# Kernel optimization log

Measured on AMD Instinct MI355X. Metric: run time of the kernel, lower is better.

## Reference

```python
import jax, jax.numpy as jnp
import numpy as np

N_NODES = 50000
N_EDGES = 800000
IN_C = 256
HID_C = 256
OUT_C = 128
N_GRAPHS = 256


def setup_inputs() -> dict:
    key = jax.random.key(0)
    ks = jax.random.split(key, 12)
    x = jax.random.normal(ks[0], (N_NODES, IN_C), dtype=jnp.float32)
    src = jax.random.randint(ks[1], (N_EDGES,), 0, N_NODES, dtype=jnp.int32)
    dst = jnp.sort(jax.random.randint(ks[2], (N_EDGES,), 0, N_NODES, dtype=jnp.int32))
    p = jax.random.uniform(ks[3], (N_NODES,), dtype=jnp.float32)
    batch = jnp.sort(jax.random.randint(ks[4], (N_NODES,), 0, N_GRAPHS, dtype=jnp.int32))
    root_ptr = jax.random.randint(ks[5], (N_GRAPHS,), 0, N_NODES, dtype=jnp.int32)
    s1 = 1.0 / np.sqrt(IN_C)
    s2 = 1.0 / np.sqrt(HID_C)
    s3 = 1.0 / np.sqrt(2 * HID_C)
    Wl1 = jax.random.uniform(ks[6], (IN_C, HID_C), jnp.float32, -s1, s1)
    Wr1 = jax.random.uniform(ks[7], (IN_C, HID_C), jnp.float32, -s1, s1)
    b1 = jnp.zeros((HID_C,), jnp.float32)
    Wl2 = jax.random.uniform(ks[8], (HID_C, HID_C), jnp.float32, -s2, s2)
    Wr2 = jax.random.uniform(ks[9], (HID_C, HID_C), jnp.float32, -s2, s2)
    b2 = jnp.zeros((HID_C,), jnp.float32)
    Wlin = jax.random.uniform(ks[10], (2 * HID_C, OUT_C), jnp.float32, -s3, s3)
    blin = jax.random.uniform(ks[11], (OUT_C,), jnp.float32, -s3, s3)
    return {"x": x, "src": src, "dst": dst, "p": p, "batch": batch,
            "root_ptr": root_ptr, "num_graphs": N_GRAPHS,
            "Wl1": Wl1, "Wr1": Wr1, "b1": b1,
            "Wl2": Wl2, "Wr2": Wr2, "b2": b2,
            "Wlin": Wlin, "blin": blin}


def _sage_conv(x, src, dst, inv_deg, Wl, Wr, b):
    # mean aggregation of neighbor features: scatter-add then divide by degree
    agg = jax.ops.segment_sum(x[src], dst, num_segments=N_NODES)  # [N, d]
    agg = agg * inv_deg[:, None]
    return agg @ Wl + x @ Wr + b


def reference(x, src, dst, p, batch, root_ptr, num_graphs,
              Wl1, Wr1, b1, Wl2, Wr2, b2, Wlin, blin):
    # in-degree for mean aggregation (shared by both convs)
    deg = jax.ops.segment_sum(jnp.ones_like(dst, dtype=x.dtype), dst,
                              num_segments=N_NODES)
    inv_deg = jnp.where(deg > 0, 1.0 / jnp.maximum(deg, 1.0), 0.0)

    h = _sage_conv(x, src, dst, inv_deg, Wl1, Wr1, b1)
    h = jax.nn.relu(h)  # dropout is identity in eval mode
    h = _sage_conv(h, src, dst, inv_deg, Wl2, Wr2, b2)

    # masked mean pool of p-weighted features per graph
    pw = h * p[:, None]
    gsum = jax.ops.segment_sum(pw, batch, num_segments=num_graphs)
    gcnt = jax.ops.segment_sum(jnp.ones_like(p), batch, num_segments=num_graphs)
    gmean = gsum / jnp.maximum(gcnt, 1.0)[:, None]

    feat = jnp.concatenate([h[root_ptr], gmean], axis=-1)  # [G, 2*hid]
    return feat @ Wlin + blin
```

## Files before the change

kernel.cpp:

```cpp
#include <hip/hip_runtime.h>
#include <hip/hip_bf16.h>

#define N_NODES 50000
#define N_EDGES 800000
#define C_DIM   256
#define OUT_C   128
#define N_GRAPHS 256

typedef unsigned short ushort8 __attribute__((ext_vector_type(8)));
typedef __bf16         bf16x8  __attribute__((ext_vector_type(8)));
typedef float          f32x4   __attribute__((ext_vector_type(4)));

typedef __attribute__((address_space(1))) const unsigned int gu32;
typedef __attribute__((address_space(3))) unsigned int lu32;

#if __has_builtin(__builtin_amdgcn_sched_barrier)
#define SCHED_FENCE() __builtin_amdgcn_sched_barrier(0)
#else
#define SCHED_FENCE() ((void)0)
#endif

__device__ __forceinline__ float us2f(unsigned short u) {
    unsigned int x = ((unsigned int)u) << 16;
    return __builtin_bit_cast(float, x);
}
__device__ __forceinline__ unsigned short f2bf(float f) {
    unsigned int u = __builtin_bit_cast(unsigned int, f);
    u += 0x7fffu + ((u >> 16) & 1u);
    return (unsigned short)(u >> 16);
}

__device__ __forceinline__ int lower_bound_i(const int* __restrict__ a, int n, int v) {
    int lo = 0, hi = n;
    while (lo < hi) {
        int mid = (lo + hi) >> 1;
        if (a[mid] < v) lo = mid + 1; else hi = mid;
    }
    return lo;
}

__global__ void preprocess(const float* __restrict__ x, unsigned short* __restrict__ xb,
                           const float* __restrict__ W0, const float* __restrict__ W1,
                           const float* __restrict__ W2, const float* __restrict__ W3,
                           unsigned short* __restrict__ D0, unsigned short* __restrict__ D1,
                           unsigned short* __restrict__ D2, unsigned short* __restrict__ D3,
                           const int* __restrict__ dst, const int* __restrict__ batch,
                           int* __restrict__ row_ptr, int* __restrict__ graph_ptr,
                           float* __restrict__ inv_deg) {
    __shared__ float tile[64][65];
    int b = blockIdx.x;
    int t = threadIdx.x;
    if (b < 12500) {
        int i = b * 256 + t;
        float4 v = *(const float4*)(x + ((size_t)i << 2));
        ushort4 o;
        o.x = f2bf(v.x); o.y = f2bf(v.y); o.z = f2bf(v.z); o.w = f2bf(v.w);
        *(ushort4*)(xb + ((size_t)i << 2)) = o;
    } else if (b < 12564) {
        int b2 = b - 12500;
        const float* S; unsigned short* D;
        switch (b2 >> 4) {
            case 0: S = W0; D = D0; break;
            case 1: S = W1; D = D1; break;
            case 2: S = W2; D = D2; break;
            default: S = W3; D = D3; break;
        }
        int tl = b2 & 15;
        int kt = (tl >> 2) * 64, nt = (tl & 3) * 64;
#pragma unroll
        for (int j = 0; j < 16; ++j) {
            int idx = t + j * 256;
            int r = idx >> 6, c = idx & 63;
            tile[r][c] = S[(size_t)(kt + r) * 256 + nt + c];
        }
        __syncthreads();
#pragma unroll
        for (int j = 0; j < 16; ++j) {
            int idx = t + j * 256;
            int r = idx >> 6, c = idx & 63;
            D[(size_t)(nt + r) * 256 + kt + c] = f2bf(tile[c][r]);
        }
    } else {
        int i = (b - 12564) * 256 + t;
        if (i <= N_NODES) {
            int lb = lower_bound_i(dst, N_EDGES, i);
            row_ptr[i] = lb;
            if (i < N_NODES) {
                int ub = lower_bound_i(dst, N_EDGES, i + 1);
                int cnt = ub - lb;
                inv_deg[i] = (cnt > 0) ? (1.0f / (float)cnt) : 0.0f;
            }
        }
        if (i <= N_GRAPHS) graph_ptr[i] = lower_bound_i(batch, N_NODES, i);
    }
}

__global__ void aggregate(const unsigned short* __restrict__ X,
                          const int* __restrict__ src,
                          const int* __restrict__ row_ptr,
                          const float* __restrict__ inv_deg,
                          unsigned short* __restrict__ out) {
    int gw   = (blockIdx.x * blockDim.x + threadIdx.x) >> 6;
    int lane = threadIdx.x & 63;
    if (gw >= N_NODES) return;
    int e0 = row_ptr[gw], e1 = row_ptr[gw + 1];
    const int lo = lane << 2;
    float a0 = 0.f, a1 = 0.f, a2 = 0.f, a3 = 0.f;
    int e = e0;

    for (; e + 16 <= e1; e += 16) {
        ushort4 v[16];
#pragma unroll
        for (int j = 0; j < 16; ++j) {
            int s = __builtin_amdgcn_readfirstlane(src[e + j]);
            v[j] = *(const ushort4*)(X + ((size_t)s << 8) + lo);
        }
        SCHED_FENCE();
#pragma unroll
        for (int j = 0; j < 16; ++j) {
            a0 += us2f(v[j].x); a1 += us2f(v[j].y);
            a2 += us2f(v[j].z); a3 += us2f(v[j].w);
        }
    }
    int rem = e1 - e;
    if (rem > 0) {
        int cl = e1 - 1;
        ushort4 v[16]; float w[16];
#pragma unroll
        for (int j = 0; j < 16; ++j) {
            int ej = e + j;
            int ec = ej < cl ? ej : cl;
            w[j] = (ej < e1) ? 1.0f : 0.0f;
            int s = __builtin_amdgcn_readfirstlane(src[ec]);
            v[j] = *(const ushort4*)(X + ((size_t)s << 8) + lo);
        }
        SCHED_FENCE();
#pragma unroll
        for (int j = 0; j < 16; ++j) {
            a0 = fmaf(us2f(v[j].x), w[j], a0);
            a1 = fmaf(us2f(v[j].y), w[j], a1);
            a2 = fmaf(us2f(v[j].z), w[j], a2);
            a3 = fmaf(us2f(v[j].w), w[j], a3);
        }
    }

    float sc = inv_deg[gw];
    ushort4 o;
    o.x = f2bf(a0 * sc); o.y = f2bf(a1 * sc); o.z = f2bf(a2 * sc); o.w = f2bf(a3 * sc);
    *(ushort4*)(out + ((size_t)gw << 8) + lo) = o;
}

__global__ __launch_bounds__(512, 2)
void gemm_fused(const unsigned short* __restrict__ A1,
                const unsigned short* __restrict__ A2,
                const unsigned short* __restrict__ B1t,
                const unsigned short* __restrict__ B2t,
                const float* __restrict__ bias,
                unsigned short* __restrict__ C,
                int M, int do_relu) {
    __shared__ __align__(16) unsigned short As[8192];
    __shared__ __align__(16) unsigned short Bs[16384];

    const int t    = threadIdx.x;
    const int m0   = blockIdx.x * 128;
    const int lane = t & 63, wid = t >> 6;
    const int wm   = (wid >> 2) * 64;
    const int wn   = (wid & 3) * 64;
    const int lrow = lane & 15;
    const int kq   = lane >> 4;

    const f32x4 zero4 = {0.f, 0.f, 0.f, 0.f};
    f32x4 acc[4][4];
#pragma unroll
    for (int i = 0; i < 4; ++i)
#pragma unroll
        for (int j = 0; j < 4; ++j) acc[i][j] = zero4;

    for (int it = 0; it < 8; ++it) {
        const unsigned short* __restrict__ Ab = (it < 4) ? A1 : A2;
        const unsigned short* __restrict__ Bb = (it < 4) ? B1t : B2t;
        int ko = (it * 64) & 255;

#pragma unroll
        for (int i = 0; i < 2; ++i) {
            int q   = t + i * 512;
            int row = q >> 3;
            int kb  = (q & 7) ^ (row & 7);
            const unsigned short* ga = Ab + (size_t)(m0 + row) * 256 + ko + kb * 8;
            __builtin_amdgcn_global_load_lds((gu32*)ga, (lu32*)(As + q * 8), 16, 0, 0);
        }
#pragma unroll
        for (int i = 0; i < 4; ++i) {
            int q   = t + i * 512;
            int row = q >> 3;
            int kb  = (q & 7) ^ (row & 7);
            const unsigned short* gb = Bb + (size_t)row * 256 + ko + kb * 8;
            __builtin_amdgcn_global_load_lds((gu32*)gb, (lu32*)(Bs + q * 8), 16, 0, 0);
        }
        __syncthreads();

#pragma unroll
        for (int s = 0; s < 2; ++s) {
            int kqp = s * 4 + kq;
            bf16x8 af[4], bfr[4];
#pragma unroll
            for (int mi = 0; mi < 4; ++mi) {
                int r = wm + mi * 16 + lrow;
                int slot = r * 8 + (kqp ^ (lrow & 7));
                uint4 u = *(const uint4*)(As + slot * 8);
                af[mi] = __builtin_bit_cast(bf16x8, u);
            }
#pragma unroll
            for (int ni = 0; ni < 4; ++ni) {
                int r = wn + ni * 16 + lrow;
                int slot = r * 8 + (kqp ^ (lrow & 7));
                uint4 u = *(const uint4*)(Bs + slot * 8);
                bfr[ni] = __builtin_bit_cast(bf16x8, u);
            }
#pragma unroll
            for (int mi = 0; mi < 4; ++mi)
#pragma unroll
                for (int ni = 0; ni < 4; ++ni)
                    acc[mi][ni] = __builtin_amdgcn_mfma_f32_16x16x32_bf16(
                        af[mi], bfr[ni], acc[mi][ni], 0, 0, 0);
        }
        __syncthreads();
    }

    const int rbase = (lane >> 4) * 4;
#pragma unroll
    for (int ni = 0; ni < 4; ++ni) {
        int n  = wn + ni * 16 + lrow;
        float bv = bias[n];
#pragma unroll
        for (int mi = 0; mi < 4; ++mi) {
            int mb = m0 + wm + mi * 16 + rbase;
#pragma unroll
            for (int r = 0; r < 4; ++r) {
                int m = mb + r;
                if (m < M) {
                    float v = acc[mi][ni][r] + bv;
                    if (do_relu) v = fmaxf(v, 0.f);
                    C[(size_t)m * 256 + n] = f2bf(v);
                }
            }
        }
    }
}

__global__ void pool_final(const unsigned short* __restrict__ h2,
                           const float* __restrict__ p,
                           const int* __restrict__ graph_ptr,
                           const int* __restrict__ root_ptr,
                           const float* __restrict__ Wlin,
                           const float* __restrict__ blin,
                           float* __restrict__ out) {
    __shared__ float part[2][256];
    __shared__ float fl[512];
    int g = blockIdx.x;
    int t = threadIdx.x;
    int c = t & 255;
    int half = t >> 8;
    int s = graph_ptr[g], e = graph_ptr[g + 1];
    int mid = s + ((e - s) >> 1);
    int lo0 = half ? mid : s;
    int hi0 = half ? e : mid;

    float acc = 0.f;
    for (int n = lo0; n < hi0; n += 8) {
        int cl = hi0 - 1;
        float w[8]; unsigned short v[8];
#pragma unroll
        for (int j = 0; j < 8; ++j) {
            int nj = n + j;
            int ncj = nj < cl ? nj : cl;
            int nu = __builtin_amdgcn_readfirstlane(ncj);
            w[j] = (nj < hi0) ? p[nu] : 0.0f;
            v[j] = h2[(size_t)nu * 256 + c];
        }
        SCHED_FENCE();
#pragma unroll
        for (int j = 0; j < 8; ++j)
            acc = fmaf(us2f(v[j]), w[j], acc);
    }
    part[half][c] = acc;
    __syncthreads();

    if (half == 0) {
        float cnt = (float)(e - s);
        int root = root_ptr[g];
        fl[c]       = us2f(h2[(size_t)root * 256 + c]);
        fl[256 + c] = (part[0][c] + part[1][c]) / fmaxf(cnt, 1.0f);
    }
    __syncthreads();

    if (t < 128) {
        int o = t;
        float s0 = 0.f, s1 = 0.f, s2 = 0.f, s3 = 0.f;
        for (int k = 0; k < 512; k += 4) {
            s0 = fmaf(fl[k + 0], Wlin[(k + 0) * 128 + o], s0);
            s1 = fmaf(fl[k + 1], Wlin[(k + 1) * 128 + o], s1);
            s2 = fmaf(fl[k + 2], Wlin[(k + 2) * 128 + o], s2);
            s3 = fmaf(fl[k + 3], Wlin[(k + 3) * 128 + o], s3);
        }
        out[(size_t)g * 128 + o] = blin[o] + ((s0 + s1) + (s2 + s3));
    }
}

extern "C" void kernel_launch(void* const* d_in, const int* in_sizes, int n_in,
                              void* d_out, int out_size, void* d_ws, size_t ws_size,
                              hipStream_t stream) {
    const float* x        = (const float*)d_in[0];
    const int*   src      = (const int*)d_in[1];
    const int*   dst      = (const int*)d_in[2];
    const float* p        = (const float*)d_in[3];
    const int*   batch    = (const int*)d_in[4];
    const int*   root_ptr = (const int*)d_in[5];
    const float* Wl1  = (const float*)d_in[7];
    const float* Wr1  = (const float*)d_in[8];
    const float* b1   = (const float*)d_in[9];
    const float* Wl2  = (const float*)d_in[10];
    const float* Wr2  = (const float*)d_in[11];
    const float* b2   = (const float*)d_in[12];
    const float* Wlin = (const float*)d_in[13];
    const float* blin = (const float*)d_in[14];
    float* out = (float*)d_out;

    size_t off = 0;
    char* base = (char*)d_ws;
    auto alloc = [&](size_t bytes) -> void* {
        void* q = base + off;
        off += (bytes + 255) & ~(size_t)255;
        return q;
    };
    int*            row_ptr   = (int*)  alloc((N_NODES + 1) * sizeof(int));
    int*            graph_ptr = (int*)  alloc((N_GRAPHS + 1) * sizeof(int));
    float*          inv_deg   = (float*)alloc(N_NODES * sizeof(float));
    unsigned short* Wl1t = (unsigned short*)alloc(256 * 256 * 2);
    unsigned short* Wr1t = (unsigned short*)alloc(256 * 256 * 2);
    unsigned short* Wl2t = (unsigned short*)alloc(256 * 256 * 2);
    unsigned short* Wr2t = (unsigned short*)alloc(256 * 256 * 2);
    unsigned short* xb   = (unsigned short*)alloc((size_t)N_NODES * 256 * 2);
    unsigned short* aggb = (unsigned short*)alloc((size_t)N_NODES * 256 * 2);
    unsigned short* h1   = (unsigned short*)alloc((size_t)N_NODES * 256 * 2);
    unsigned short* h2   = (unsigned short*)alloc((size_t)N_NODES * 256 * 2);
    (void)ws_size; (void)n_in; (void)in_sizes; (void)out_size;

    preprocess<<<12760, 256, 0, stream>>>(x, xb, Wl1, Wr1, Wl2, Wr2,
                                          Wl1t, Wr1t, Wl2t, Wr2t,
                                          dst, batch, row_ptr, graph_ptr, inv_deg);

    dim3 ggrid((N_NODES + 127) / 128);

    aggregate<<<N_NODES / 4, 256, 0, stream>>>(xb, src, row_ptr, inv_deg, aggb);
    gemm_fused<<<ggrid, 512, 0, stream>>>(aggb, xb, Wl1t, Wr1t, b1, h1, N_NODES, 1);

    aggregate<<<N_NODES / 4, 256, 0, stream>>>(h1, src, row_ptr, inv_deg, aggb);
    gemm_fused<<<ggrid, 512, 0, stream>>>(aggb, h1, Wl2t, Wr2t, b2, h2, N_NODES, 0);

    pool_final<<<N_GRAPHS, 512, 0, stream>>>(h2, p, graph_ptr, root_ptr,
                                             Wlin, blin, out);
}
```

Baseline: 314.4 us.

## Fuse graph mean-pool into second GEMM epilogue via LDS and global atomics

The second SAGE GEMM epilogue now accumulates p-weighted outputs per graph into a small LDS buffer, then flushes them with global atomics into a zeroed gsum buffer. This removes the separate pass in pool_final that re-read all of h2. The x-conversion branch of preprocess now handles four vectors per thread, and extra blocks zero gsum. The fusion relies on each 128-row tile spanning at most 8 graphs, and it adds LDS atomic traffic and extra LDS usage to the GEMM epilogue.

```diff
diff --git a/kernel.cpp b/kernel.cpp
--- a/kernel.cpp
+++ b/kernel.cpp
@@ -7,7 +7,6 @@
 #define OUT_C   128
 #define N_GRAPHS 256
 
-typedef unsigned short ushort8 __attribute__((ext_vector_type(8)));
 typedef __bf16         bf16x8  __attribute__((ext_vector_type(8)));
 typedef float          f32x4   __attribute__((ext_vector_type(4)));
 
@@ -46,18 +45,22 @@
                            unsigned short* __restrict__ D2, unsigned short* __restrict__ D3,
                            const int* __restrict__ dst, const int* __restrict__ batch,
                            int* __restrict__ row_ptr, int* __restrict__ graph_ptr,
-                           float* __restrict__ inv_deg) {
+                           float* __restrict__ inv_deg, float* __restrict__ gsum) {
     __shared__ float tile[64][65];
     int b = blockIdx.x;
     int t = threadIdx.x;
-    if (b < 12500) {
-        int i = b * 256 + t;
-        float4 v = *(const float4*)(x + ((size_t)i << 2));
-        ushort4 o;
-        o.x = f2bf(v.x); o.y = f2bf(v.y); o.z = f2bf(v.z); o.w = f2bf(v.w);
-        *(ushort4*)(xb + ((size_t)i << 2)) = o;
-    } else if (b < 12564) {
-        int b2 = b - 12500;
+    if (b < 3125) {
+        int base = b * 1024 + t;
+#pragma unroll
+        for (int j = 0; j < 4; ++j) {
+            int i = base + j * 256;
+            float4 v = *(const float4*)(x + ((size_t)i << 2));
+            ushort4 o;
+            o.x = f2bf(v.x); o.y = f2bf(v.y); o.z = f2bf(v.z); o.w = f2bf(v.w);
+            *(ushort4*)(xb + ((size_t)i << 2)) = o;
+        }
+    } else if (b < 3189) {
+        int b2 = b - 3125;
         const float* S; unsigned short* D;
         switch (b2 >> 4) {
             case 0: S = W0; D = D0; break;
@@ -80,8 +83,8 @@
             int r = idx >> 6, c = idx & 63;
             D[(size_t)(nt + r) * 256 + kt + c] = f2bf(tile[c][r]);
         }
-    } else {
-        int i = (b - 12564) * 256 + t;
+    } else if (b < 3385) {
+        int i = (b - 3189) * 256 + t;
         if (i <= N_NODES) {
             int lb = lower_bound_i(dst, N_EDGES, i);
             row_ptr[i] = lb;
@@ -92,6 +95,10 @@
             }
         }
         if (i <= N_GRAPHS) graph_ptr[i] = lower_bound_i(batch, N_NODES, i);
+    } else {
+        int i = (b - 3385) * 256 + t;
+        f32x4 z = {0.f, 0.f, 0.f, 0.f};
+        ((f32x4*)gsum)[i] = z;
     }
 }
 
@@ -157,9 +164,13 @@
                 const unsigned short* __restrict__ B2t,
                 const float* __restrict__ bias,
                 unsigned short* __restrict__ C,
-                int M, int do_relu) {
+                int M, int do_relu,
+                const float* __restrict__ p,
+                const int* __restrict__ batch,
+                float* __restrict__ gsum, int do_pool) {
     __shared__ __align__(16) unsigned short As[8192];
     __shared__ __align__(16) unsigned short Bs[16384];
+    __shared__ float pool_lds[8][256];
 
     const int t    = threadIdx.x;
     const int m0   = blockIdx.x * 128;
@@ -169,6 +180,10 @@
     const int lrow = lane & 15;
     const int kq   = lane >> 4;
 
+    if (do_pool) {
+        for (int i = t; i < 2048; i += 512) ((float*)pool_lds)[i] = 0.f;
+    }
+
     const f32x4 zero4 = {0.f, 0.f, 0.f, 0.f};
     f32x4 acc[4][4];
 #pragma unroll
@@ -228,83 +243,75 @@
     }
 
     const int rbase = (lane >> 4) * 4;
-#pragma unroll
-    for (int ni = 0; ni < 4; ++ni) {
-        int n  = wn + ni * 16 + lrow;
-        float bv = bias[n];
-#pragma unroll
-        for (int mi = 0; mi < 4; ++mi) {
-            int mb = m0 + wm + mi * 16 + rbase;
-#pragma unroll
-            for (int r = 0; r < 4; ++r) {
-                int m = mb + r;
-                if (m < M) {
-                    float v = acc[mi][ni][r] + bv;
+    const int gfirst = do_pool ? batch[m0] : 0;
+    float bv[4];
+#pragma unroll
+    for (int ni = 0; ni < 4; ++ni) bv[ni] = bias[wn + ni * 16 + lrow];
+
+#pragma unroll
+    for (int mi = 0; mi < 4; ++mi) {
+#pragma unroll
+        for (int r = 0; r < 4; ++r) {
+            int m = m0 + wm + mi * 16 + rbase + r;
+            if (m < M) {
+                float pwv = 0.f; int slot = 0;
+                if (do_pool) {
+                    pwv  = p[m];
+                    slot = (batch[m] - gfirst) & 7;
+                }
+#pragma unroll
+                for (int ni = 0; ni < 4; ++ni) {
+                    int n = wn + ni * 16 + lrow;
+                    float v = acc[mi][ni][r] + bv[ni];
                     if (do_relu) v = fmaxf(v, 0.f);
                     C[(size_t)m * 256 + n] = f2bf(v);
+                    if (do_pool) atomicAdd(&pool_lds[slot][n], pwv * v);
                 }
             }
         }
     }
+
+    if (do_pool) {
+        __syncthreads();
+        for (int i = t; i < 2048; i += 512) {
+            int slot = i >> 8, n = i & 255;
+            float v2 = ((float*)pool_lds)[i];
+            int g = gfirst + slot;
+            if (v2 != 0.f && g < N_GRAPHS)
+                atomicAdd(&gsum[g * 256 + n], v2);
+        }
+    }
 }
 
 __global__ void pool_final(const unsigned short* __restrict__ h2,
-                           const float* __restrict__ p,
                            const int* __restrict__ graph_ptr,
                            const int* __restrict__ root_ptr,
+                           const float* __restrict__ gsum,
                            const float* __restrict__ Wlin,
                            const float* __restrict__ blin,
                            float* __restrict__ out) {
-    __shared__ float part[2][256];
     __shared__ float fl[512];
     int g = blockIdx.x;
     int t = threadIdx.x;
-    int c = t & 255;
-    int half = t >> 8;
     int s = graph_ptr[g], e = graph_ptr[g + 1];
-    int mid = s + ((e - s) >> 1);
-    int lo0 = half ? mid : s;
-    int hi0 = half ? e : mid;
-
-    float acc = 0.f;
-    for (int n = lo0; n < hi0; n += 8) {
-        int cl = hi0 - 1;
-        float w[8]; unsigned short v[8];
-#pragma unroll
-        for (int j = 0; j < 8; ++j) {
-            int nj = n + j;
-            int ncj = nj < cl ? nj : cl;
-            int nu = __builtin_amdgcn_readfirstlane(ncj);
-            w[j] = (nj < hi0) ? p[nu] : 0.0f;
-            v[j] = h2[(size_t)nu * 256 + c];
-        }
-        SCHED_FENCE();
-#pragma unroll
-        for (int j = 0; j < 8; ++j)
-            acc = fmaf(us2f(v[j]), w[j], acc);
-    }
-    part[half][c] = acc;
+    float icnt = 1.0f / fmaxf((float)(e - s), 1.0f);
+    int root = root_ptr[g];
+#pragma unroll
+    for (int c = t; c < 256; c += 128) {
+        fl[c]       = us2f(h2[(size_t)root * 256 + c]);
+        fl[256 + c] = gsum[g * 256 + c] * icnt;
+    }
     __syncthreads();
 
-    if (half == 0) {
-        float cnt = (float)(e - s);
-        int root = root_ptr[g];
-        fl[c]       = us2f(h2[(size_t)root * 256 + c]);
-        fl[256 + c] = (part[0][c] + part[1][c]) / fmaxf(cnt, 1.0f);
-    }
-    __syncthreads();
-
-    if (t < 128) {
-        int o = t;
-        float s0 = 0.f, s1 = 0.f, s2 = 0.f, s3 = 0.f;
-        for (int k = 0; k < 512; k += 4) {
-            s0 = fmaf(fl[k + 0], Wlin[(k + 0) * 128 + o], s0);
-            s1 = fmaf(fl[k + 1], Wlin[(k + 1) * 128 + o], s1);
-            s2 = fmaf(fl[k + 2], Wlin[(k + 2) * 128 + o], s2);
-            s3 = fmaf(fl[k + 3], Wlin[(k + 3) * 128 + o], s3);
-        }
-        out[(size_t)g * 128 + o] = blin[o] + ((s0 + s1) + (s2 + s3));
-    }
+    int o = t;
+    float s0 = 0.f, s1 = 0.f, s2 = 0.f, s3 = 0.f;
+    for (int k = 0; k < 512; k += 4) {
+        s0 = fmaf(fl[k + 0], Wlin[(k + 0) * 128 + o], s0);
+        s1 = fmaf(fl[k + 1], Wlin[(k + 1) * 128 + o], s1);
+        s2 = fmaf(fl[k + 2], Wlin[(k + 2) * 128 + o], s2);
+        s3 = fmaf(fl[k + 3], Wlin[(k + 3) * 128 + o], s3);
+    }
+    out[(size_t)g * 128 + o] = blin[o] + ((s0 + s1) + (s2 + s3));
 }
 
 extern "C" void kernel_launch(void* const* d_in, const int* in_sizes, int n_in,
@@ -336,6 +343,7 @@
     int*            row_ptr   = (int*)  alloc((N_NODES + 1) * sizeof(int));
     int*            graph_ptr = (int*)  alloc((N_GRAPHS + 1) * sizeof(int));
     float*          inv_deg   = (float*)alloc(N_NODES * sizeof(float));
+    float*          gsum      = (float*)alloc((size_t)N_GRAPHS * 256 * sizeof(float));
     unsigned short* Wl1t = (unsigned short*)alloc(256 * 256 * 2);
     unsigned short* Wr1t = (unsigned short*)alloc(256 * 256 * 2);
     unsigned short* Wl2t = (unsigned short*)alloc(256 * 256 * 2);
@@ -346,18 +354,21 @@
     unsigned short* h2   = (unsigned short*)alloc((size_t)N_NODES * 256 * 2);
     (void)ws_size; (void)n_in; (void)in_sizes; (void)out_size;
 
-    preprocess<<<12760, 256, 0, stream>>>(x, xb, Wl1, Wr1, Wl2, Wr2,
-                                          Wl1t, Wr1t, Wl2t, Wr2t,
-                                          dst, batch, row_ptr, graph_ptr, inv_deg);
+    preprocess<<<3449, 256, 0, stream>>>(x, xb, Wl1, Wr1, Wl2, Wr2,
+                                         Wl1t, Wr1t, Wl2t, Wr2t,
+                                         dst, batch, row_ptr, graph_ptr, inv_deg,
+                                         gsum);
 
     dim3 ggrid((N_NODES + 127) / 128);
 
     aggregate<<<N_NODES / 4, 256, 0, stream>>>(xb, src, row_ptr, inv_deg, aggb);
-    gemm_fused<<<ggrid, 512, 0, stream>>>(aggb, xb, Wl1t, Wr1t, b1, h1, N_NODES, 1);
+    gemm_fused<<<ggrid, 512, 0, stream>>>(aggb, xb, Wl1t, Wr1t, b1, h1, N_NODES, 1,
+                                          p, batch, gsum, 0);
 
     aggregate<<<N_NODES / 4, 256, 0, stream>>>(h1, src, row_ptr, inv_deg, aggb);
-    gemm_fused<<<ggrid, 512, 0, stream>>>(aggb, h1, Wl2t, Wr2t, b2, h2, N_NODES, 0);
-
-    pool_final<<<N_GRAPHS, 512, 0, stream>>>(h2, p, graph_ptr, root_ptr,
+    gemm_fused<<<ggrid, 512, 0, stream>>>(aggb, h1, Wl2t, Wr2t, b2, h2, N_NODES, 0,
+                                          p, batch, gsum, 1);
+
+    pool_final<<<N_GRAPHS, 128, 0, stream>>>(h2, graph_ptr, root_ptr, gsum,
                                              Wlin, blin, out);
 }
```

Result: slower. 372.8 us (+18.6%).
